# Performance work log

Hardware: AMD Instinct MI355X
Metric: run time of the kernel (lower is better)

Reference implementation:

```python
import jax, jax.numpy as jnp
import numpy as np

CUTOFF = 0.5
MARGIN = 0.2
BETA_VAL = 1.2
DIST_EPS = 1e-4  # p_dist clamp(min=eps) before sqrt
PAIR_EPS = 1e-8  # added inside triplet distance sqrt


def setup_inputs() -> dict:
    key = jax.random.key(0)
    k1, k2, k3, k4 = jax.random.split(key, 4)
    B, D, C = 4096, 512, 100
    x = jax.random.normal(k1, (B, D), dtype=jnp.float32)
    batch = x / jnp.linalg.norm(x, axis=1, keepdims=True)  # unit sphere, as sampler assumes
    labels = jax.random.randint(k2, (B,), 0, C)
    beta = jnp.ones((C,), dtype=jnp.float32) * BETA_VAL
    gumbel_pos = jax.random.gumbel(k3, (B, B), dtype=jnp.float32)
    gumbel_neg = jax.random.gumbel(k4, (B, B), dtype=jnp.float32)
    return {"batch": batch, "beta": beta, "gumbel_pos": gumbel_pos,
            "gumbel_neg": gumbel_neg, "labels": labels}


def reference(batch, beta, gumbel_pos, gumbel_neg, labels):
    B, D = batch.shape
    # --- distance-weighted sampling (detached in original) ---
    xb = jax.lax.stop_gradient(batch)
    prod = xb @ xb.T                                   # [B,B]
    sq = jnp.diagonal(prod)
    d2 = jnp.clip(sq[:, None] + sq[None, :] - 2.0 * prod, 0.0)
    dist = jnp.sqrt(jnp.clip(d2, DIST_EPS))
    dist = jnp.clip(dist, CUTOFF)                      # distances.clamp(min=cutoff)
    same = labels[:, None] == labels[None, :]          # [B,B]
    # log q_d^{-1}(d) = (2-D) log d - (D-3)/2 log(1 - d^2/4)
    log_q = (2.0 - D) * jnp.log(dist) - (D - 3) / 2.0 * jnp.log(1.0 - 0.25 * dist * dist)
    neg_logits = jnp.where(same, -jnp.inf, log_q)      # same-class prob zeroed
    # Gumbel-max == categorical with p \propto exp(log_q) (normalization cancels)
    neg_idx = jnp.argmax(neg_logits + gumbel_neg, axis=1)
    pos_mask = same & ~jnp.eye(B, dtype=bool)          # same label, excluding self
    pos_idx = jnp.argmax(jnp.where(pos_mask, gumbel_pos, -jnp.inf), axis=1)
    # --- margin triplet loss ---
    d_ap = jnp.sqrt(jnp.sum((batch - batch[pos_idx]) ** 2, axis=1) + PAIR_EPS)
    d_an = jnp.sqrt(jnp.sum((batch - batch[neg_idx]) ** 2, axis=1) + PAIR_EPS)
    b = beta[labels]
    pos_loss = jax.nn.relu(d_ap - b + MARGIN)
    neg_loss = jax.nn.relu(b - d_an + MARGIN)
    pair_count = jnp.sum((pos_loss > 0).astype(jnp.float32) + (neg_loss > 0).astype(jnp.float32))
    total = jnp.sum(pos_loss + neg_loss)
    return jnp.where(pair_count == 0.0, total, total / pair_count)
```

## Files before the change

kernel.cpp:

```cpp
#include <hip/hip_runtime.h>
#include <math.h>

#define B_N 4096
#define D_DIM 512
#define MARGIN 0.2f
#define PAIR_EPS 1e-8f
#define NEG_INF (-INFINITY)

typedef __attribute__((ext_vector_type(8))) short bf16x8;
typedef __attribute__((ext_vector_type(4))) float f32x4;

constexpr size_t WS_SQ   = 0x1000;
constexpr size_t WS_XH   = 0x10000;
constexpr size_t WS_XL   = 0x410000;
constexpr size_t WS_PART = 0x810000;

__device__ __forceinline__ unsigned short f2bf(float f) {
  unsigned int u = __float_as_uint(f);
  unsigned int r = (u + 0x7fffu + ((u >> 16) & 1u)) >> 16;
  return (unsigned short)r;
}
__device__ __forceinline__ float bf2f(unsigned short h) {
  return __uint_as_float(((unsigned int)h) << 16);
}

typedef __attribute__((address_space(1))) const void* gptr_t;
typedef __attribute__((address_space(3))) void* lptr_t;
__device__ __forceinline__ void gload_lds16(const void* g, void* l) {
  __builtin_amdgcn_global_load_lds((gptr_t)g, (lptr_t)l, 16, 0, 0);
}

__global__ __launch_bounds__(256) void k_prep(const float* __restrict__ batch,
                                              float* __restrict__ accum,
                                              float* __restrict__ sq,
                                              unsigned short* __restrict__ xh,
                                              unsigned short* __restrict__ xl) {
  if (blockIdx.x == 0 && threadIdx.x == 0) { accum[0] = 0.f; accum[1] = 0.f; }
  int row  = blockIdx.x * 4 + (threadIdx.x >> 6);
  int lane = threadIdx.x & 63;
  const size_t base = (size_t)row * D_DIM;
  float s = 0.f;
#pragma unroll
  for (int e = 0; e < 2; ++e) {
    const int off = lane * 4 + e * 256;
    float4 v = *(const float4*)(batch + base + off);
    ushort4 h, l;
    h.x = f2bf(v.x); l.x = f2bf(v.x - bf2f(h.x));
    h.y = f2bf(v.y); l.y = f2bf(v.y - bf2f(h.y));
    h.z = f2bf(v.z); l.z = f2bf(v.z - bf2f(h.z));
    h.w = f2bf(v.w); l.w = f2bf(v.w - bf2f(h.w));
    *(ushort4*)(xh + base + off) = h;
    *(ushort4*)(xl + base + off) = l;
    s += v.x * v.x + v.y * v.y + v.z * v.z + v.w * v.w;
  }
#pragma unroll
  for (int off = 32; off; off >>= 1) s += __shfl_xor(s, off);
  if (lane == 0) sq[row] = s;
}

__global__ __launch_bounds__(512, 2) void k_gemm(
    const unsigned short* __restrict__ Xh, const unsigned short* __restrict__ Xl,
    const float* __restrict__ gpos, const float* __restrict__ gneg,
    const int* __restrict__ labels, const float* __restrict__ sq,
    float4* __restrict__ part) {
  __shared__ unsigned short As[2][256 * 64];
  __shared__ unsigned short Bs[2][256 * 64];
  __shared__ float s_sqi[256], s_sqj[256];
  __shared__ int   s_lbi[256], s_lbj[256];

  const int jb = blockIdx.x, ib = blockIdx.y;
  const int i0 = ib * 256, j0 = jb * 256;
  const int tid = threadIdx.x;
  const int w = tid >> 6, lane = tid & 63;
  const int wm = w & 1, wn = w >> 1;
  const int lr = lane & 15;
  const int lk = (lane >> 4) * 8;

  if (tid < 256)      { s_sqi[tid] = sq[i0 + tid];       s_lbi[tid] = labels[i0 + tid]; }
  else                { int t = tid - 256; s_sqj[t] = sq[j0 + t]; s_lbj[t] = labels[j0 + t]; }

  f32x4 acc[8][4] = {};

  const int srow = lane >> 3;
  const int scol = (((lane & 7) ^ (lane >> 3)) << 3);

#define STAGE(c, t)                                                              \
  {                                                                              \
    const int p_ = (t) >> 3;                                                     \
    const unsigned short* Asrc = (p_ < 2) ? Xh : Xl;                             \
    const unsigned short* Bsrc = (p_ == 1) ? Xl : Xh;                            \
    const int kk_ = ((t) & 7) * 64;                                              \
    _Pragma("unroll")                                                            \
    for (int q = 0; q < 4; ++q) {                                                \
      const int row = q * 64 + w * 8 + srow;                                     \
      gload_lds16(Asrc + ((size_t)(i0 + row) << 9) + kk_ + scol,                 \
                  &As[c][q * 4096 + w * 512]);                                   \
      gload_lds16(Bsrc + ((size_t)(j0 + row) << 9) + kk_ + scol,                 \
                  &Bs[c][q * 4096 + w * 512]);                                   \
    }                                                                            \
  }

  STAGE(0, 0);
  __syncthreads();

  int cur = 0;
  for (int t = 0; t < 24; ++t) {
    if (t + 1 < 24) STAGE(cur ^ 1, t + 1);
    const char* Ab = (const char*)&As[cur][0];
    const char* Bb = (const char*)&Bs[cur][0];
#pragma unroll
    for (int kk2 = 0; kk2 < 64; kk2 += 32) {
      bf16x8 af[8], bfv[4];
#pragma unroll
      for (int mi = 0; mi < 8; ++mi) {
        const int row = wm * 128 + mi * 16 + lr;
        const int byt = ((row << 7) + ((kk2 + lk) << 1)) ^ ((lane & 7) << 4);
        af[mi] = *(const bf16x8*)(Ab + byt);
      }
#pragma unroll
      for (int ni = 0; ni < 4; ++ni) {
        const int row = wn * 64 + ni * 16 + lr;
        const int byt = ((row << 7) + ((kk2 + lk) << 1)) ^ ((lane & 7) << 4);
        bfv[ni] = *(const bf16x8*)(Bb + byt);
      }
      __builtin_amdgcn_s_setprio(1);
#pragma unroll
      for (int mi = 0; mi < 8; ++mi)
#pragma unroll
        for (int ni = 0; ni < 4; ++ni)
          acc[mi][ni] = __builtin_amdgcn_mfma_f32_16x16x32_bf16(af[mi], bfv[ni], acc[mi][ni], 0, 0, 0);
      __builtin_amdgcn_s_setprio(0);
    }
    __syncthreads();
    cur ^= 1;
  }

  float4* red = (float4*)&As[0][0];
#pragma unroll
  for (int mi = 0; mi < 8; ++mi) {
#pragma unroll
    for (int r = 0; r < 4; ++r) {
      const int lrow = wm * 128 + mi * 16 + ((lane >> 4) << 2) + r;
      const int gi = i0 + lrow;
      const int li = s_lbi[lrow];
      const float sqi = s_sqi[lrow];
      float nv = NEG_INF; int nix = 0;
      float pv = NEG_INF; int pix = 0;
#pragma unroll
      for (int ni = 0; ni < 4; ++ni) {
        const int cj = wn * 64 + ni * 16 + lr;
        const int gj = j0 + cj;
        const float g = acc[mi][ni][r];
        float d2 = sqi + s_sqj[cj] - 2.f * g;
        float e2 = fmaxf(d2, 0.25f);
        float lq = -255.f * __logf(e2) - 254.5f * __logf(1.f - 0.25f * e2);
        const bool same = (li == s_lbj[cj]);
        float cn = same ? NEG_INF : lq + gneg[(size_t)gi * B_N + gj];
        if (cn > nv) { nv = cn; nix = gj; }
        float cp = NEG_INF;
        if (same & (gi != gj)) cp = gpos[(size_t)gi * B_N + gj];
        if (cp > pv) { pv = cp; pix = gj; }
      }
#pragma unroll
      for (int off = 1; off < 16; off <<= 1) {
        float onv = __shfl_xor(nv, off); int onix = __shfl_xor(nix, off);
        if (onv > nv || (onv == nv && onix < nix)) { nv = onv; nix = onix; }
        float opv = __shfl_xor(pv, off); int opix = __shfl_xor(pix, off);
        if (opv > pv || (opv == pv && opix < pix)) { pv = opv; pix = opix; }
      }
      if (lr == 0) red[lrow * 4 + wn] = make_float4(nv, __int_as_float(nix), pv, __int_as_float(pix));
    }
  }
  __syncthreads();
  if (tid < 256) {
    float nv = NEG_INF, pv = NEG_INF; int nix = 0, pix = 0;
#pragma unroll
    for (int q = 0; q < 4; ++q) {
      float4 e = red[tid * 4 + q];
      int eni = __float_as_int(e.y), epi = __float_as_int(e.w);
      if (e.x > nv || (e.x == nv && eni < nix)) { nv = e.x; nix = eni; }
      if (e.z > pv || (e.z == pv && epi < pix)) { pv = e.z; pix = epi; }
    }
    part[((size_t)(ib * 16 + jb)) * 256 + tid] =
        make_float4(nv, __int_as_float(nix), pv, __int_as_float(pix));
  }
#undef STAGE
}

__global__ __launch_bounds__(512) void k_reduce(const float* __restrict__ batch,
                                                const float* __restrict__ beta,
                                                const int* __restrict__ labels,
                                                const float4* __restrict__ part,
                                                float* __restrict__ accum) {
  __shared__ float2 s_bsum[8];
  const int wave = threadIdx.x >> 6, lane = threadIdx.x & 63;
  const int row = blockIdx.x * 8 + wave;
  float nv = NEG_INF, pv = NEG_INF;
  int nix = 0x7fffffff, pix = 0x7fffffff;
  if (lane < 16) {
    float4 p = part[((size_t)(row >> 8) * 16 + lane) * 256 + (row & 255)];
    nv = p.x; nix = __float_as_int(p.y);
    pv = p.z; pix = __float_as_int(p.w);
  }
#pragma unroll
  for (int off = 8; off; off >>= 1) {
    float onv = __shfl_xor(nv, off); int onix = __shfl_xor(nix, off);
    if (onv > nv || (onv == nv && onix < nix)) { nv = onv; nix = onix; }
    float opv = __shfl_xor(pv, off); int opix = __shfl_xor(pix, off);
    if (opv > pv || (opv == pv && opix < pix)) { pv = opv; pix = opix; }
  }
  nix = __shfl(nix, 0); pix = __shfl(pix, 0);

  const float* xi = batch + (size_t)row * D_DIM;
  const float* xp = batch + (size_t)pix * D_DIM;
  const float* xn = batch + (size_t)nix * D_DIM;
  float sap = 0.f, san = 0.f;
#pragma unroll
  for (int e = 0; e < 2; ++e) {
    float4 a = ((const float4*)xi)[lane * 2 + e];
    float4 p = ((const float4*)xp)[lane * 2 + e];
    float4 n = ((const float4*)xn)[lane * 2 + e];
    float dx = a.x - p.x, dy = a.y - p.y, dz = a.z - p.z, dw = a.w - p.w;
    sap += dx * dx + dy * dy + dz * dz + dw * dw;
    dx = a.x - n.x; dy = a.y - n.y; dz = a.z - n.z; dw = a.w - n.w;
    san += dx * dx + dy * dy + dz * dz + dw * dw;
  }
#pragma unroll
  for (int off = 32; off; off >>= 1) {
    sap += __shfl_xor(sap, off);
    san += __shfl_xor(san, off);
  }
  if (lane == 0) {
    float d_ap = sqrtf(sap + PAIR_EPS);
    float d_an = sqrtf(san + PAIR_EPS);
    float b = beta[labels[row]];
    float pl = fmaxf(d_ap - b + MARGIN, 0.f);
    float nl = fmaxf(b - d_an + MARGIN, 0.f);
    float cnt = (pl > 0.f ? 1.f : 0.f) + (nl > 0.f ? 1.f : 0.f);
    s_bsum[wave] = make_float2(pl + nl, cnt);
  }
  __syncthreads();
  if (threadIdx.x == 0) {
    float tot = 0.f, cnt = 0.f;
#pragma unroll
    for (int q = 0; q < 8; ++q) { tot += s_bsum[q].x; cnt += s_bsum[q].y; }
    atomicAdd(&accum[0], tot);
    atomicAdd(&accum[1], cnt);
  }
}

__global__ void k_final(const float* __restrict__ accum, float* __restrict__ out) {
  float tot = accum[0], cnt = accum[1];
  out[0] = (cnt == 0.f) ? tot : tot / cnt;
}

extern "C" void kernel_launch(void* const* d_in, const int* in_sizes, int n_in,
                              void* d_out, int out_size, void* d_ws, size_t ws_size,
                              hipStream_t stream) {
  const float* batch  = (const float*)d_in[0];
  const float* beta   = (const float*)d_in[1];
  const float* gpos   = (const float*)d_in[2];
  const float* gneg   = (const float*)d_in[3];
  const int*   labels = (const int*)d_in[4];
  float* out = (float*)d_out;

  float*          accum = (float*)d_ws;
  float*          sq    = (float*)((char*)d_ws + WS_SQ);
  unsigned short* xh    = (unsigned short*)((char*)d_ws + WS_XH);
  unsigned short* xl    = (unsigned short*)((char*)d_ws + WS_XL);
  float4*         part  = (float4*)((char*)d_ws + WS_PART);

  k_prep<<<B_N / 4, 256, 0, stream>>>(batch, accum, sq, xh, xl);
  dim3 g(16, 16);
  k_gemm<<<g, 512, 0, stream>>>(xh, xl, gpos, gneg, labels, sq, part);
  k_reduce<<<B_N / 8, 512, 0, stream>>>(batch, beta, labels, part, accum);
  k_final<<<1, 1, 0, stream>>>(accum, out);
}
```

Before: 290.1 us.

## Interleave global-to-LDS prefetch with MFMA phases using fine-grained waitcnt barriers

Restructures the GEMM main loop into four sub-phases per K-tile. Each phase loads a slice of A fragments, issues part of the next tile's global-to-LDS loads, and runs its MFMAs. Explicit vmcnt/lgkmcnt waits and raw s_barriers replace the full __syncthreads, so memory traffic overlaps compute more evenly. This adds more barriers per iteration, and the hand-counted vmcnt values are a correctness risk if the load ordering changes.

```diff
diff --git a/kernel.cpp b/kernel.cpp
--- a/kernel.cpp
+++ b/kernel.cpp
@@ -84,56 +84,84 @@
   const int srow = lane >> 3;
   const int scol = (((lane & 7) ^ (lane >> 3)) << 3);
 
-#define STAGE(c, t)                                                              \
-  {                                                                              \
-    const int p_ = (t) >> 3;                                                     \
-    const unsigned short* Asrc = (p_ < 2) ? Xh : Xl;                             \
-    const unsigned short* Bsrc = (p_ == 1) ? Xl : Xh;                            \
-    const int kk_ = ((t) & 7) * 64;                                              \
-    _Pragma("unroll")                                                            \
-    for (int q = 0; q < 4; ++q) {                                                \
-      const int row = q * 64 + w * 8 + srow;                                     \
-      gload_lds16(Asrc + ((size_t)(i0 + row) << 9) + kk_ + scol,                 \
-                  &As[c][q * 4096 + w * 512]);                                   \
-      gload_lds16(Bsrc + ((size_t)(j0 + row) << 9) + kk_ + scol,                 \
-                  &Bs[c][q * 4096 + w * 512]);                                   \
-    }                                                                            \
-  }
-
-  STAGE(0, 0);
-  __syncthreads();
-
-  int cur = 0;
+#define STG_A(src, kk, np, qq)                                                    \
+  gload_lds16((src) + (((size_t)(i0 + (qq) * 64 + w * 8 + srow) << 9) + (kk) + scol), \
+              &As[np][(qq) * 4096 + w * 512])
+#define STG_B(src, kk, np, qq)                                                    \
+  gload_lds16((src) + (((size_t)(j0 + (qq) * 64 + w * 8 + srow) << 9) + (kk) + scol), \
+              &Bs[np][(qq) * 4096 + w * 512])
+
+  STG_B(Xh, 0, 0, 0); STG_B(Xh, 0, 0, 1); STG_B(Xh, 0, 0, 2); STG_B(Xh, 0, 0, 3);
+  STG_A(Xh, 0, 0, 0); STG_A(Xh, 0, 0, 2);
+  STG_A(Xh, 0, 0, 1); STG_A(Xh, 0, 0, 3);
+  asm volatile("s_waitcnt vmcnt(2)" ::: "memory");
+  __builtin_amdgcn_s_barrier();
+
+#pragma unroll 1
   for (int t = 0; t < 24; ++t) {
-    if (t + 1 < 24) STAGE(cur ^ 1, t + 1);
-    const char* Ab = (const char*)&As[cur][0];
-    const char* Bb = (const char*)&Bs[cur][0];
-#pragma unroll
-    for (int kk2 = 0; kk2 < 64; kk2 += 32) {
-      bf16x8 af[8], bfv[4];
-#pragma unroll
-      for (int mi = 0; mi < 8; ++mi) {
-        const int row = wm * 128 + mi * 16 + lr;
-        const int byt = ((row << 7) + ((kk2 + lk) << 1)) ^ ((lane & 7) << 4);
-        af[mi] = *(const bf16x8*)(Ab + byt);
-      }
-#pragma unroll
-      for (int ni = 0; ni < 4; ++ni) {
-        const int row = wn * 64 + ni * 16 + lr;
-        const int byt = ((row << 7) + ((kk2 + lk) << 1)) ^ ((lane & 7) << 4);
-        bfv[ni] = *(const bf16x8*)(Bb + byt);
-      }
+    const int c = t & 1;
+    const char* Ab = (const char*)&As[c][0];
+    const char* Bb = (const char*)&Bs[c][0];
+    const int n  = t + 1;
+    const int np = n & 1;
+    const int pn = n >> 3;
+    const unsigned short* nA = (pn < 2) ? Xh : Xl;
+    const unsigned short* nB = (pn == 1) ? Xl : Xh;
+    const int nkk = (n & 7) * 64;
+
+    bf16x8 bfv[4][2];
+#pragma unroll
+    for (int q = 0; q < 4; ++q) {
+      bf16x8 af[2][2];
+#pragma unroll
+      for (int ml = 0; ml < 2; ++ml) {
+        const int row = wm * 128 + (2 * q + ml) * 16 + lr;
+#pragma unroll
+        for (int kx = 0; kx < 2; ++kx) {
+          const int byt = ((row << 7) + ((kx * 32 + lk) << 1)) ^ ((lane & 7) << 4);
+          af[ml][kx] = *(const bf16x8*)(Ab + byt);
+        }
+      }
+      if (q == 0) {
+#pragma unroll
+        for (int ni = 0; ni < 4; ++ni) {
+          const int row = wn * 64 + ni * 16 + lr;
+#pragma unroll
+          for (int kx = 0; kx < 2; ++kx) {
+            const int byt = ((row << 7) + ((kx * 32 + lk) << 1)) ^ ((lane & 7) << 4);
+            bfv[ni][kx] = *(const bf16x8*)(Bb + byt);
+          }
+        }
+      }
+      if (n < 24) {
+        if (q == 0)      { STG_B(nB, nkk, np, 0); STG_B(nB, nkk, np, 1); }
+        else if (q == 1) { STG_B(nB, nkk, np, 2); STG_B(nB, nkk, np, 3); }
+        else if (q == 2) { STG_A(nA, nkk, np, 0); STG_A(nA, nkk, np, 2); }
+        else             { STG_A(nA, nkk, np, 1); STG_A(nA, nkk, np, 3); }
+      }
+      __builtin_amdgcn_s_barrier();
+      asm volatile("s_waitcnt lgkmcnt(0)" ::: "memory");
+      __builtin_amdgcn_sched_barrier(0);
       __builtin_amdgcn_s_setprio(1);
 #pragma unroll
-      for (int mi = 0; mi < 8; ++mi)
-#pragma unroll
-        for (int ni = 0; ni < 4; ++ni)
-          acc[mi][ni] = __builtin_amdgcn_mfma_f32_16x16x32_bf16(af[mi], bfv[ni], acc[mi][ni], 0, 0, 0);
+      for (int kx = 0; kx < 2; ++kx)
+#pragma unroll
+        for (int ml = 0; ml < 2; ++ml)
+#pragma unroll
+          for (int ni = 0; ni < 4; ++ni)
+            acc[2 * q + ml][ni] = __builtin_amdgcn_mfma_f32_16x16x32_bf16(
+                af[ml][kx], bfv[ni][kx], acc[2 * q + ml][ni], 0, 0, 0);
       __builtin_amdgcn_s_setprio(0);
+      if (q == 1) {
+        if (t < 23) asm volatile("s_waitcnt vmcnt(4)" ::: "memory");
+        else        asm volatile("s_waitcnt vmcnt(0)" ::: "memory");
+      }
+      if (q == 3) asm volatile("s_waitcnt vmcnt(2)" ::: "memory");
+      __builtin_amdgcn_s_barrier();
     }
-    __syncthreads();
-    cur ^= 1;
-  }
+  }
+#undef STG_A
+#undef STG_B
 
   float4* red = (float4*)&As[0][0];
 #pragma unroll
@@ -184,7 +212,6 @@
     part[((size_t)(ib * 16 + jb)) * 256 + tid] =
         make_float4(nv, __int_as_float(nix), pv, __int_as_float(pix));
   }
-#undef STAGE
 }
 
 __global__ __launch_bounds__(512) void k_reduce(const float* __restrict__ batch,
```

Result: no change. 291.9 us (+0.6%).
